# Kernel optimization log

Hardware: AMD Instinct MI355X
Metric: run time of the kernel (lower is better)

## Reference

```python
import jax, jax.numpy as jnp
import numpy as np

OBS = 256      # observation_space_size == state_vector_len
SV = 2047      # STATE_VECTORS = WMG_MAX_OBS
D = 256        # tfm_vec_size = 8 heads * 32 head_size
H = 8
HD = 32
L = 2          # TFM_NUM_LAYERS
FF = 1024      # TFM_HIDDEN_SIZE
ACH = 512      # AC_HIDDEN_LAYER_SIZE
A = 16         # action_space_size


def setup_inputs() -> dict:
    key = jax.random.key(0)
    ks = jax.random.split(key, 24)
    r = lambda k, s: (jax.random.normal(k, s, jnp.float32) * 0.02)
    inp = {
        "observation": jax.random.normal(ks[0], (OBS,), jnp.float32),
        "old_vectors": jax.random.normal(ks[1], (SV, OBS), jnp.float32),
        "W_core": r(ks[2], (OBS, D)), "b_core": jnp.zeros((D,), jnp.float32),
        # memo embedding takes cat(state_vec, age_onehot) of size OBS+SV
        "W_memo": r(ks[3], (OBS + SV, D)), "b_memo": jnp.zeros((D,), jnp.float32),
        "Wq": r(ks[4], (L, D, D)), "bq": jnp.zeros((L, D), jnp.float32),
        "Wk": r(ks[5], (L, D, D)), "bk": jnp.zeros((L, D), jnp.float32),
        "Wv": r(ks[6], (L, D, D)), "bv": jnp.zeros((L, D), jnp.float32),
        "Wo": r(ks[7], (L, D, D)), "bo": jnp.zeros((L, D), jnp.float32),
        "ln1_g": jnp.ones((L, D), jnp.float32), "ln1_b": jnp.zeros((L, D), jnp.float32),
        "ln2_g": jnp.ones((L, D), jnp.float32), "ln2_b": jnp.zeros((L, D), jnp.float32),
        "W_ff1": r(ks[8], (L, D, FF)), "b_ff1": jnp.zeros((L, FF), jnp.float32),
        "W_ff2": r(ks[9], (L, FF, D)), "b_ff2": jnp.zeros((L, D), jnp.float32),
        "aW1": r(ks[10], (D, ACH)), "ab1": jnp.zeros((ACH,), jnp.float32),
        "aW2": r(ks[11], (ACH, ACH)), "ab2": jnp.zeros((ACH,), jnp.float32),
        "aWo": r(ks[12], (ACH, A)), "abo": jnp.zeros((A,), jnp.float32),
        "cW1": r(ks[13], (D, ACH)), "cb1": jnp.zeros((ACH,), jnp.float32),
        "cW2": r(ks[14], (ACH, ACH)), "cb2": jnp.zeros((ACH,), jnp.float32),
        "cWo": r(ks[15], (ACH, 1)), "cbo": jnp.zeros((1,), jnp.float32),
    }
    return inp


def _ln(x, g, b, eps=1e-5):
    m = jnp.mean(x, axis=-1, keepdims=True)
    v = jnp.mean(jnp.square(x - m), axis=-1, keepdims=True)
    return (x - m) * jax.lax.rsqrt(v + eps) * g + b


def reference(observation, old_vectors, W_core, b_core, W_memo, b_memo,
              Wq, bq, Wk, bk, Wv, bv, Wo, bo,
              ln1_g, ln1_b, ln2_g, ln2_b, W_ff1, b_ff1, W_ff2, b_ff2,
              aW1, ab1, aW2, ab2, aWo, abo, cW1, cb1, cW2, cb2, cWo, cbo):
    # core embedding [D]
    emb0 = observation @ W_core + b_core
    # fused memo + age-onehot embedding: cat(vec_i, e_i) @ W_memo == vec_i @ W_memo[:OBS] + W_memo[OBS+i]
    memo_emb = old_vectors @ W_memo[:OBS] + W_memo[OBS:] + b_memo  # [SV, D]
    x = jnp.concatenate([emb0[None, :], memo_emb], axis=0)[None]   # [1, 1+SV, D]
    S = 1 + SV
    scale = 1.0 / np.sqrt(HD).astype(np.float32)
    for l in range(L):
        q = (x @ Wq[l] + bq[l]).reshape(1, S, H, HD)
        k = (x @ Wk[l] + bk[l]).reshape(1, S, H, HD)
        v = (x @ Wv[l] + bv[l]).reshape(1, S, H, HD)
        scores = jnp.einsum('bqhd,bkhd->bhqk', q, k) * scale       # [1,H,S,S]
        probs = jax.nn.softmax(scores, axis=-1)
        ctx = jnp.einsum('bhqk,bkhd->bqhd', probs, v).reshape(1, S, D)
        x = _ln(x + ctx @ Wo[l] + bo[l], ln1_g[l], ln1_b[l])
        h = jax.nn.gelu(x @ W_ff1[l] + b_ff1[l])
        x = _ln(x + h @ W_ff2[l] + b_ff2[l], ln2_g[l], ln2_b[l])
    t = x[:, 0, :]                                                 # [1, D]
    ha = jnp.tanh(jnp.tanh(t @ aW1 + ab1) @ aW2 + ab2)
    policy = ha @ aWo + abo                                        # [1, A] logits
    hc = jnp.tanh(jnp.tanh(t @ cW1 + cb1) @ cW2 + cb2)
    value_est = hc @ cWo + cbo                                     # [1, 1]
    # WMG_MAX_MEMOS == 0 path: new state vector is tanh(observation)
    new_vector = jnp.tanh(observation)                             # [OBS]
    return value_est, policy, new_vector
```

## Files before the change

kernel.cpp:

```cpp
#include <hip/hip_runtime.h>
#include <stdint.h>

typedef __attribute__((ext_vector_type(8))) short bf16x8;
typedef __attribute__((ext_vector_type(4))) float f32x4;

constexpr int kOBS = 256;
constexpr int kSEQ = 2048;
constexpr int kD   = 256;
constexpr int kHD  = 32;
constexpr int kFF  = 1024;
constexpr int kACH = 512;
constexpr int kA   = 16;

__device__ __forceinline__ unsigned short f2b(float f) {
  union { float f; unsigned int u; } v; v.f = f;
  unsigned int r = v.u + 0x7FFFu + ((v.u >> 16) & 1u);
  return (unsigned short)(r >> 16);
}

struct ConvTable {
  const float* src[14];
  int K[14];
  int N[14];
  int dst[14];
  int tstart[15];
};

__global__ __launch_bounds__(256) void k_convert(ConvTable tab,
                                                 unsigned short* __restrict__ wT) {
  __shared__ unsigned short lt[64][72];
  int b = blockIdx.x;
  int m = 0;
  while (b >= tab.tstart[m + 1]) m++;
  const int tloc = b - tab.tstart[m];
  const int N = tab.N[m], K = tab.K[m];
  const int ntile = N >> 6;
  const int k0 = (tloc / ntile) * 64, n0 = (tloc % ntile) * 64;
  const float* src = tab.src[m];
  const int tid = threadIdx.x;
  {
    const int r = tid >> 2, c16 = (tid & 3) * 16;
    const float* sp = src + (size_t)(k0 + r) * N + n0 + c16;
    #pragma unroll
    for (int j = 0; j < 16; j++) lt[r][c16 + j] = f2b(sp[j]);
  }
  __syncthreads();
  {
    const int n = tid >> 2, kc = (tid & 3) * 16;
    unsigned short* dp = wT + tab.dst[m] + (size_t)(n0 + n) * K + k0 + kc;
    unsigned short g[16];
    #pragma unroll
    for (int j = 0; j < 16; j++) g[j] = lt[kc + j][n];
    *(bf16x8*)dp = *(bf16x8*)&g[0];
    *(bf16x8*)(dp + 8) = *(bf16x8*)&g[8];
  }
}

__global__ __launch_bounds__(256) void k_row0(const float* __restrict__ obs,
                                              const float* __restrict__ Wc,
                                              const float* __restrict__ bc,
                                              float* __restrict__ xf,
                                              unsigned short* __restrict__ xb) {
  const int n = threadIdx.x;
  float a = bc[n];
  #pragma unroll 8
  for (int k = 0; k < kOBS; k++) a += obs[k] * Wc[k * kD + n];
  xf[n] = a;
  xb[n] = f2b(a);
}

template <int EPI, bool AF32>
__global__ __launch_bounds__(256) void k_gemmA(
    const void* __restrict__ Ap, int lda, int M, int K,
    const unsigned short* __restrict__ BT,
    const float* __restrict__ p0, const float* __restrict__ p1,
    const float* __restrict__ p2,
    void* __restrict__ o0, void* __restrict__ o1, void* __restrict__ o2) {
  __shared__ unsigned short Al[64][40];
  __shared__ unsigned short Bl[64][40];
  const int tid = threadIdx.x;
  const int w = tid >> 6, l = tid & 63, lg = l >> 4, lr = l & 15;
  const int m0 = blockIdx.x * 64, n0 = blockIdx.y * 64;
  const int sr = tid >> 2, sk = (tid & 3) * 8;
  f32x4 acc[4];
  #pragma unroll
  for (int c = 0; c < 4; c++)
    #pragma unroll
    for (int i = 0; i < 4; i++) acc[c][i] = 0.f;

  auto loadA = [&](int k0) -> bf16x8 {
    bf16x8 av;
    if (m0 + sr < M) {
      if constexpr (AF32) {
        const float* ap = (const float*)Ap + (size_t)(m0 + sr) * lda + k0 + sk;
        #pragma unroll
        for (int j = 0; j < 8; j++) av[j] = (short)f2b(ap[j]);
      } else {
        av = *(const bf16x8*)((const unsigned short*)Ap +
                              (size_t)(m0 + sr) * lda + k0 + sk);
      }
    } else {
      #pragma unroll
      for (int j = 0; j < 8; j++) av[j] = 0;
    }
    return av;
  };

  bf16x8 av = loadA(0);
  bf16x8 bv = *(const bf16x8*)(BT + (size_t)(n0 + sr) * K + sk);

  for (int k0 = 0; k0 < K; k0 += 32) {
    __syncthreads();
    *(bf16x8*)&Al[sr][sk] = av;
    *(bf16x8*)&Bl[sr][sk] = bv;
    __syncthreads();
    if (k0 + 32 < K) {
      av = loadA(k0 + 32);
      bv = *(const bf16x8*)(BT + (size_t)(n0 + sr) * K + k0 + 32 + sk);
    }
    bf16x8 af = *(bf16x8*)&Al[w * 16 + lr][8 * lg];
    #pragma unroll
    for (int c = 0; c < 4; c++) {
      bf16x8 bf = *(bf16x8*)&Bl[c * 16 + lr][8 * lg];
      acc[c] = __builtin_amdgcn_mfma_f32_16x16x32_bf16(af, bf, acc[c], 0, 0, 0);
    }
  }

  #pragma unroll
  for (int c = 0; c < 4; c++) {
    #pragma unroll
    for (int i = 0; i < 4; i++) {
      const int gr = m0 + w * 16 + 4 * lg + i;
      const int gc = n0 + c * 16 + lr;
      if (gr >= M) continue;
      float v = acc[c][i];
      if constexpr (EPI == 0) {
        v += p0[gc] + p1[(size_t)gr * kD + gc];
        ((float*)o0)[(size_t)(gr + 1) * kD + gc] = v;
        ((unsigned short*)o1)[(size_t)(gr + 1) * kD + gc] = f2b(v);
      } else if constexpr (EPI == 1) {
        const int t = gc >> 8, cc = gc & 255;
        const float* bp = (t == 0) ? p0 : (t == 1 ? p1 : p2);
        unsigned short* op = (t == 0) ? (unsigned short*)o0
                              : (t == 1 ? (unsigned short*)o1
                                        : (unsigned short*)o2);
        v += bp[cc];
        if (t == 0) v *= 0.17677669529663687f;
        op[(size_t)gr * kD + cc] = f2b(v);
      } else if constexpr (EPI == 2) {
        v += p0[gc];
        const float g =
            0.5f * v *
            (1.0f + tanhf(0.7978845608028654f * (v + 0.044715f * v * v * v)));
        ((unsigned short*)o0)[(size_t)gr * kFF + gc] = f2b(g);
      } else {
        v += p0[gc] + ((const float*)o1)[(size_t)gr * kD + gc];
        ((float*)o0)[(size_t)gr * kD + gc] = v;
      }
    }
  }
}

__global__ __launch_bounds__(256) void k_ln(const float* __restrict__ tin,
                                            const float* __restrict__ gam,
                                            const float* __restrict__ bet,
                                            float* __restrict__ xf,
                                            unsigned short* __restrict__ xb) {
  const int w = threadIdx.x >> 6, l = threadIdx.x & 63;
  const int row = blockIdx.x * 4 + w;
  f32x4 v = *(const f32x4*)(tin + (size_t)row * kD + l * 4);
  float s = v[0] + v[1] + v[2] + v[3];
  #pragma unroll
  for (int mm = 1; mm < 64; mm <<= 1) s += __shfl_xor(s, mm);
  const float mn = s * (1.0f / 256.0f);
  const float d0 = v[0] - mn, d1 = v[1] - mn, d2 = v[2] - mn, d3 = v[3] - mn;
  float s2 = d0 * d0 + d1 * d1 + d2 * d2 + d3 * d3;
  #pragma unroll
  for (int mm = 1; mm < 64; mm <<= 1) s2 += __shfl_xor(s2, mm);
  const float rstd = rsqrtf(s2 * (1.0f / 256.0f) + 1e-5f);
  f32x4 g4 = *(const f32x4*)(gam + l * 4);
  f32x4 b4 = *(const f32x4*)(bet + l * 4);
  f32x4 y;
  y[0] = d0 * rstd * g4[0] + b4[0];
  y[1] = d1 * rstd * g4[1] + b4[1];
  y[2] = d2 * rstd * g4[2] + b4[2];
  y[3] = d3 * rstd * g4[3] + b4[3];
  *(f32x4*)(xf + (size_t)row * kD + l * 4) = y;
  unsigned long long pk = (unsigned long long)f2b(y[0]) |
                          ((unsigned long long)f2b(y[1]) << 16) |
                          ((unsigned long long)f2b(y[2]) << 32) |
                          ((unsigned long long)f2b(y[3]) << 48);
  *(unsigned long long*)(xb + (size_t)row * kD + l * 4) = pk;
}

__global__ __launch_bounds__(256) void k_attn(const unsigned short* __restrict__ q,
                                              const unsigned short* __restrict__ k,
                                              const unsigned short* __restrict__ v,
                                              float* __restrict__ pacc,
                                              float* __restrict__ pml,
                                              int tpb) {
  __shared__ unsigned short Kl[64][40];
  __shared__ unsigned short Vt[32][72];
  __shared__ unsigned short Pl[4][16][72];
  const int tid = threadIdx.x;
  const int w = tid >> 6, l = tid & 63, lg = l >> 4, lr = l & 15;
  const int q0 = blockIdx.x * 64;
  const int hoff = blockIdx.y * kHD;
  const int sr = tid >> 2, sk = (tid & 3) * 8;
  const int t0 = blockIdx.z * tpb;

  const bf16x8 qf =
      *(const bf16x8*)(q + (size_t)(q0 + w * 16 + lr) * kD + hoff + 8 * lg);

  float m_[4], l_[4];
  f32x4 acc[2];
  #pragma unroll
  for (int i = 0; i < 4; i++) { m_[i] = -1e30f; l_[i] = 0.f; }
  #pragma unroll
  for (int dt = 0; dt < 2; dt++)
    #pragma unroll
    for (int i = 0; i < 4; i++) acc[dt][i] = 0.f;

  bf16x8 kreg = *(const bf16x8*)(k + (size_t)(t0 * 64 + sr) * kD + hoff + sk);
  bf16x8 vreg = *(const bf16x8*)(v + (size_t)(t0 * 64 + sr) * kD + hoff + sk);

  for (int t = 0; t < tpb; t++) {
    __syncthreads();
    *(bf16x8*)&Kl[sr][sk] = kreg;
    #pragma unroll
    for (int j = 0; j < 8; j++) Vt[sk + j][sr] = (unsigned short)vreg[j];
    __syncthreads();
    if (t + 1 < tpb) {
      const size_t nx = (size_t)((t0 + t + 1) * 64 + sr) * kD + hoff + sk;
      kreg = *(const bf16x8*)(k + nx);
      vreg = *(const bf16x8*)(v + nx);
    }
    f32x4 s[4];
    #pragma unroll
    for (int c = 0; c < 4; c++) {
      f32x4 z;
      #pragma unroll
      for (int i = 0; i < 4; i++) z[i] = 0.f;
      bf16x8 kf = *(bf16x8*)&Kl[c * 16 + lr][8 * lg];
      s[c] = __builtin_amdgcn_mfma_f32_16x16x32_bf16(qf, kf, z, 0, 0, 0);
    }
    float tm[4];
    #pragma unroll
    for (int i = 0; i < 4; i++)
      tm[i] = fmaxf(fmaxf(s[0][i], s[1][i]), fmaxf(s[2][i], s[3][i]));
    #pragma unroll
    for (int mm = 1; mm <= 8; mm <<= 1)
      #pragma unroll
      for (int i = 0; i < 4; i++) tm[i] = fmaxf(tm[i], __shfl_xor(tm[i], mm));
    float p[4][4], rs[4], corr[4];
    #pragma unroll
    for (int i = 0; i < 4; i++) {
      const float nm = fmaxf(m_[i], tm[i]);
      corr[i] = __expf(m_[i] - nm);
      m_[i] = nm;
      rs[i] = 0.f;
    }
    #pragma unroll
    for (int c = 0; c < 4; c++)
      #pragma unroll
      for (int i = 0; i < 4; i++) {
        p[c][i] = __expf(s[c][i] - m_[i]);
        rs[i] += p[c][i];
      }
    #pragma unroll
    for (int mm = 1; mm <= 8; mm <<= 1)
      #pragma unroll
      for (int i = 0; i < 4; i++) rs[i] += __shfl_xor(rs[i], mm);
    #pragma unroll
    for (int i = 0; i < 4; i++) {
      l_[i] = l_[i] * corr[i] + rs[i];
      acc[0][i] *= corr[i];
      acc[1][i] *= corr[i];
    }
    #pragma unroll
    for (int c = 0; c < 4; c++)
      #pragma unroll
      for (int i = 0; i < 4; i++)
        Pl[w][4 * lg + i][c * 16 + lr] = f2b(p[c][i]);
    __syncthreads();
    #pragma unroll
    for (int k2 = 0; k2 < 2; k2++) {
      bf16x8 pf = *(bf16x8*)&Pl[w][lr][k2 * 32 + 8 * lg];
      #pragma unroll
      for (int dt = 0; dt < 2; dt++) {
        bf16x8 vf = *(bf16x8*)&Vt[dt * 16 + lr][k2 * 32 + 8 * lg];
        acc[dt] = __builtin_amdgcn_mfma_f32_16x16x32_bf16(pf, vf, acc[dt], 0, 0, 0);
      }
    }
  }

  const int pb = blockIdx.z * 8 + blockIdx.y;
  float* pa = pacc + (size_t)pb * kSEQ * kHD;
  float* pm = pml + (size_t)pb * kSEQ * 2;
  #pragma unroll
  for (int dt = 0; dt < 2; dt++)
    #pragma unroll
    for (int i = 0; i < 4; i++) {
      const int gr = q0 + w * 16 + 4 * lg + i;
      pa[(size_t)gr * kHD + dt * 16 + lr] = acc[dt][i];
    }
  if (lr == 0) {
    #pragma unroll
    for (int i = 0; i < 4; i++) {
      const int gr = q0 + w * 16 + 4 * lg + i;
      float2 ml; ml.x = m_[i]; ml.y = l_[i];
      *(float2*)&pm[(size_t)gr * 2] = ml;
    }
  }
}

__global__ __launch_bounds__(256) void k_combine(const float* __restrict__ pacc,
                                                 const float* __restrict__ pml,
                                                 unsigned short* __restrict__ ctx,
                                                 int nsplit) {
  const int tid = threadIdx.x;
  const int d = tid & 31;
  const int g = blockIdx.x * 8 + (tid >> 5);
  const int h = g >> 11;
  const int row = g & 2047;
  float M = -1e30f;
  for (int s = 0; s < nsplit; s++)
    M = fmaxf(M, pml[((size_t)(s * 8 + h) * kSEQ + row) * 2]);
  float L = 0.f, o = 0.f;
  for (int s = 0; s < nsplit; s++) {
    const size_t pb = (size_t)(s * 8 + h) * kSEQ + row;
    const float2 ml = *(const float2*)&pml[pb * 2];
    const float e = __expf(ml.x - M);
    L += ml.y * e;
    o += pacc[pb * kHD + d] * e;
  }
  ctx[(size_t)row * kD + h * kHD + d] = f2b(o / L);
}

__global__ __launch_bounds__(256) void k_head1(const float* __restrict__ xf,
                                               const float* __restrict__ aW1,
                                               const float* __restrict__ ab1,
                                               const float* __restrict__ cW1,
                                               const float* __restrict__ cb1,
                                               float* __restrict__ h1) {
  __shared__ float tl[256];
  __shared__ float red[4][64];
  const int tid = threadIdx.x;
  tl[tid] = xf[tid];
  __syncthreads();
  const int jj = blockIdx.x * 64;
  const bool actor = jj < 512;
  const float* W = actor ? aW1 : cW1;
  const float* b = actor ? ab1 : cb1;
  const int j0 = actor ? jj : jj - 512;
  const int ks = tid >> 6, j = tid & 63;
  float s = 0.f;
  #pragma unroll 4
  for (int k2 = ks * 64; k2 < ks * 64 + 64; k2++)
    s += tl[k2] * W[(size_t)k2 * kACH + j0 + j];
  red[ks][j] = s;
  __syncthreads();
  if (tid < 64) {
    float t = red[0][tid] + red[1][tid] + red[2][tid] + red[3][tid] + b[j0 + tid];
    h1[jj + tid] = tanhf(t);
  }
}

__global__ __launch_bounds__(256) void k_head2(const float* __restrict__ h1,
                                               const float* __restrict__ aW2,
                                               const float* __restrict__ ab2,
                                               const float* __restrict__ cW2,
                                               const float* __restrict__ cb2,
                                               float* __restrict__ h2) {
  __shared__ float tl[512];
  __shared__ float red[4][64];
  const int tid = threadIdx.x;
  const int jj = blockIdx.x * 64;
  const bool actor = jj < 512;
  const float* hin = actor ? h1 : h1 + 512;
  tl[tid] = hin[tid];
  tl[tid + 256] = hin[tid + 256];
  __syncthreads();
  const float* W = actor ? aW2 : cW2;
  const float* b = actor ? ab2 : cb2;
  const int j0 = actor ? jj : jj - 512;
  const int ks = tid >> 6, j = tid & 63;
  float s = 0.f;
  #pragma unroll 4
  for (int k2 = ks * 128; k2 < ks * 128 + 128; k2++)
    s += tl[k2] * W[(size_t)k2 * kACH + j0 + j];
  red[ks][j] = s;
  __syncthreads();
  if (tid < 64) {
    float t = red[0][tid] + red[1][tid] + red[2][tid] + red[3][tid] + b[j0 + tid];
    h2[jj + tid] = tanhf(t);
  }
}

__global__ __launch_bounds__(256) void k_head3(const float* __restrict__ h2,
                                               const float* __restrict__ aWo,
                                               const float* __restrict__ abo,
                                               const float* __restrict__ cWo,
                                               const float* __restrict__ cbo,
                                               const float* __restrict__ obs,
                                               float* __restrict__ out) {
  __shared__ float ha[512], hc[512], vred[4];
  const int tid = threadIdx.x;
  ha[tid] = h2[tid];
  ha[tid + 256] = h2[tid + 256];
  hc[tid] = h2[512 + tid];
  hc[tid + 256] = h2[768 + tid];
  __syncthreads();
  const int g = tid >> 4, lane16 = tid & 15;
  float s = 0.f;
  for (int k2 = lane16 * 32; k2 < lane16 * 32 + 32; k2++)
    s += ha[k2] * aWo[(size_t)k2 * kA + g];
  #pragma unroll
  for (int mm = 1; mm <= 8; mm <<= 1) s += __shfl_xor(s, mm);
  if (lane16 == 0) out[1 + g] = s + abo[g];
  float vv = hc[tid] * cWo[tid] + hc[tid + 256] * cWo[tid + 256];
  #pragma unroll
  for (int mm = 1; mm <= 32; mm <<= 1) vv += __shfl_xor(vv, mm);
  if ((tid & 63) == 0) vred[tid >> 6] = vv;
  __syncthreads();
  if (tid == 0) out[0] = vred[0] + vred[1] + vred[2] + vred[3] + cbo[0];
  out[17 + tid] = tanhf(obs[tid]);
}

extern "C" void kernel_launch(void* const* d_in, const int* in_sizes, int n_in,
                              void* d_out, int out_size, void* d_ws, size_t ws_size,
                              hipStream_t stream) {
  const float* obs   = (const float*)d_in[0];
  const float* oldv  = (const float*)d_in[1];
  const float* Wcore = (const float*)d_in[2];
  const float* bcore = (const float*)d_in[3];
  const float* Wmemo = (const float*)d_in[4];
  const float* bmemo = (const float*)d_in[5];
  const float* Wq    = (const float*)d_in[6];
  const float* bq    = (const float*)d_in[7];
  const float* Wk    = (const float*)d_in[8];
  const float* bk    = (const float*)d_in[9];
  const float* Wv    = (const float*)d_in[10];
  const float* bv    = (const float*)d_in[11];
  const float* Wo    = (const float*)d_in[12];
  const float* bo    = (const float*)d_in[13];
  const float* ln1g  = (const float*)d_in[14];
  const float* ln1b  = (const float*)d_in[15];
  const float* ln2g  = (const float*)d_in[16];
  const float* ln2b  = (const float*)d_in[17];
  const float* Wff1  = (const float*)d_in[18];
  const float* bff1  = (const float*)d_in[19];
  const float* Wff2  = (const float*)d_in[20];
  const float* bff2  = (const float*)d_in[21];
  const float* aW1   = (const float*)d_in[22];
  const float* ab1   = (const float*)d_in[23];
  const float* aW2   = (const float*)d_in[24];
  const float* ab2   = (const float*)d_in[25];
  const float* aWo   = (const float*)d_in[26];
  const float* abo   = (const float*)d_in[27];
  const float* cW1   = (const float*)d_in[28];
  const float* cb1   = (const float*)d_in[29];
  const float* cW2   = (const float*)d_in[30];
  const float* cb2   = (const float*)d_in[31];
  const float* cWo   = (const float*)d_in[32];
  const float* cbo   = (const float*)d_in[33];

  char* ws = (char*)d_ws;
  float*          xf  = (float*)(ws + 0);
  unsigned short* xb  = (unsigned short*)(ws + (2u << 20));
  unsigned short* qb  = (unsigned short*)(ws + (3u << 20));
  unsigned short* kb  = (unsigned short*)(ws + (4u << 20));
  unsigned short* vb  = (unsigned short*)(ws + (5u << 20));
  unsigned short* ctb = (unsigned short*)(ws + (6u << 20));
  unsigned short* hb  = (unsigned short*)(ws + (7u << 20));
  float*          tmp = (float*)(ws + (11u << 20));
  float*          h1  = (float*)(ws + (13u << 20));
  float*          h2  = (float*)(ws + (13u << 20) + 4096);
  unsigned short* wT  = (unsigned short*)(ws + (13u << 20) + 16384);

  const size_t pacc_off = (size_t)17u << 20;
  int nsplit = 8;
  while (nsplit > 1 &&
         pacc_off + (size_t)nsplit * (8 * kSEQ * kHD * 4 + 8 * kSEQ * 2 * 4) >
             ws_size)
    nsplit >>= 1;
  float* pacc = (float*)(ws + pacc_off);
  float* pml  = (float*)(ws + pacc_off + (size_t)nsplit * 8 * kSEQ * kHD * 4);
  const int tpb = 32 / nsplit;

  const int oCore = 0, oMemo = 65536;
  int oQKV[2], oWoT[2], oFF1[2], oFF2[2];
  int cur = 131072;
  for (int l2 = 0; l2 < 2; l2++) {
    oQKV[l2] = cur; cur += 196608;
    oWoT[l2] = cur; cur += 65536;
    oFF1[l2] = cur; cur += 262144;
    oFF2[l2] = cur; cur += 262144;
  }

  ConvTable tab;
  int idx = 0, ts = 0;
  auto add = [&](const float* s, int K, int N, int dst) {
    tab.src[idx] = s; tab.K[idx] = K; tab.N[idx] = N; tab.dst[idx] = dst;
    tab.tstart[idx] = ts; ts += (K >> 6) * (N >> 6); idx++;
  };
  add(Wcore, 256, 256, oCore);
  add(Wmemo, 256, 256, oMemo);
  for (int l2 = 0; l2 < 2; l2++) {
    add(Wq + l2 * 65536, 256, 256, oQKV[l2]);
    add(Wk + l2 * 65536, 256, 256, oQKV[l2] + 65536);
    add(Wv + l2 * 65536, 256, 256, oQKV[l2] + 131072);
    add(Wo + l2 * 65536, 256, 256, oWoT[l2]);
    add(Wff1 + l2 * 262144, 256, 1024, oFF1[l2]);
    add(Wff2 + l2 * 262144, 1024, 256, oFF2[l2]);
  }
  tab.tstart[14] = ts;

  k_row0<<<1, 256, 0, stream>>>(obs, Wcore, bcore, xf, xb);
  k_convert<<<ts, 256, 0, stream>>>(tab, wT);
  k_gemmA<0, true><<<dim3(32, 4), 256, 0, stream>>>(
      oldv, 256, 2047, 256, wT + oMemo, bmemo, Wmemo + 65536, nullptr,
      xf, xb, nullptr);

  for (int l2 = 0; l2 < 2; l2++) {
    k_gemmA<1, false><<<dim3(32, 12), 256, 0, stream>>>(
        xb, 256, 2048, 256, wT + oQKV[l2],
        bq + l2 * 256, bk + l2 * 256, bv + l2 * 256, qb, kb, vb);
    k_attn<<<dim3(32, 8, nsplit), 256, 0, stream>>>(qb, kb, vb, pacc, pml, tpb);
    k_combine<<<2048, 256, 0, stream>>>(pacc, pml, ctb, nsplit);
    k_gemmA<3, false><<<dim3(32, 4), 256, 0, stream>>>(
        ctb, 256, 2048, 256, wT + oWoT[l2],
        bo + l2 * 256, nullptr, nullptr, tmp, xf, nullptr);
    k_ln<<<512, 256, 0, stream>>>(tmp, ln1g + l2 * 256, ln1b + l2 * 256, xf, xb);
    k_gemmA<2, false><<<dim3(32, 16), 256, 0, stream>>>(
        xb, 256, 2048, 256, wT + oFF1[l2],
        bff1 + l2 * 1024, nullptr, nullptr, hb, nullptr, nullptr);
    k_gemmA<3, false><<<dim3(32, 4), 256, 0, stream>>>(
        hb, 1024, 2048, 1024, wT + oFF2[l2],
        bff2 + l2 * 256, nullptr, nullptr, tmp, xf, nullptr);
    k_ln<<<512, 256, 0, stream>>>(tmp, ln2g + l2 * 256, ln2b + l2 * 256, xf, xb);
  }

  k_head1<<<16, 256, 0, stream>>>(xf, aW1, ab1, cW1, cb1, h1);
  k_head2<<<16, 256, 0, stream>>>(h1, aW2, ab2, cW2, cb2, h2);
  k_head3<<<1, 256, 0, stream>>>(h2, aWo, abo, cWo, cbo, obs, (float*)d_out);
}
```

Before: 227.4 us.

## Fuse the whole forward pass into one cooperative persistent megakernel

Replaces the chain of about 20 kernel launches with one cooperative persistent kernel whose phases are separated by grid syncs. It also folds the split-softmax combine into the Wo GEMM and merges each LayerNorm into the preceding GEMM epilogue, so the fp32 temporaries are never written out. The attention split factor drops from 8 to 4. This is meant to remove launch gaps and intermediate memory round-trips, at the cost of grid-wide barriers, a grid capped by occupancy, and a per-kernel fallback path if the cooperative launch fails.

```diff
diff --git a/kernel.cpp b/kernel.cpp
--- a/kernel.cpp
+++ b/kernel.cpp
@@ -1,10 +1,12 @@
 #include <hip/hip_runtime.h>
+#include <hip/hip_cooperative_groups.h>
 #include <stdint.h>
+
+namespace cg = cooperative_groups;
 
 typedef __attribute__((ext_vector_type(8))) short bf16x8;
 typedef __attribute__((ext_vector_type(4))) float f32x4;
 
-constexpr int kOBS = 256;
 constexpr int kSEQ = 2048;
 constexpr int kD   = 256;
 constexpr int kHD  = 32;
@@ -26,61 +28,74 @@
   int tstart[15];
 };
 
-__global__ __launch_bounds__(256) void k_convert(ConvTable tab,
-                                                 unsigned short* __restrict__ wT) {
-  __shared__ unsigned short lt[64][72];
-  int b = blockIdx.x;
-  int m = 0;
-  while (b >= tab.tstart[m + 1]) m++;
-  const int tloc = b - tab.tstart[m];
-  const int N = tab.N[m], K = tab.K[m];
-  const int ntile = N >> 6;
-  const int k0 = (tloc / ntile) * 64, n0 = (tloc % ntile) * 64;
-  const float* src = tab.src[m];
-  const int tid = threadIdx.x;
-  {
-    const int r = tid >> 2, c16 = (tid & 3) * 16;
-    const float* sp = src + (size_t)(k0 + r) * N + n0 + c16;
-    #pragma unroll
-    for (int j = 0; j < 16; j++) lt[r][c16 + j] = f2b(sp[j]);
-  }
-  __syncthreads();
-  {
-    const int n = tid >> 2, kc = (tid & 3) * 16;
-    unsigned short* dp = wT + tab.dst[m] + (size_t)(n0 + n) * K + k0 + kc;
-    unsigned short g[16];
-    #pragma unroll
-    for (int j = 0; j < 16; j++) g[j] = lt[kc + j][n];
-    *(bf16x8*)dp = *(bf16x8*)&g[0];
-    *(bf16x8*)(dp + 8) = *(bf16x8*)&g[8];
-  }
-}
-
-__global__ __launch_bounds__(256) void k_row0(const float* __restrict__ obs,
-                                              const float* __restrict__ Wc,
-                                              const float* __restrict__ bc,
-                                              float* __restrict__ xf,
-                                              unsigned short* __restrict__ xb) {
-  const int n = threadIdx.x;
-  float a = bc[n];
-  #pragma unroll 8
-  for (int k = 0; k < kOBS; k++) a += obs[k] * Wc[k * kD + n];
-  xf[n] = a;
-  xb[n] = f2b(a);
+union SharedU {
+  struct { unsigned short lt[64][72]; } cv;
+  struct { unsigned short Al[64][40]; unsigned short Bl[64][40]; } g64;
+  struct { unsigned short Kl[64][40]; unsigned short Vt[32][72];
+           unsigned short Pl[4][16][72]; } at;
+  struct { unsigned short As[16][264]; float2 red[4][16]; } lg;
+  struct { float tl[512]; float red[4][64]; } hd;
+  struct { float ha[512]; float hc[512]; float vred[4]; } h3;
+};
+
+struct MegaParams {
+  ConvTable tab;
+  const float *obs, *oldv, *Wcore, *bcore, *bmemo, *Wmemo2;
+  const float *bq, *bk, *bv, *bo, *ln1g, *ln1b, *ln2g, *ln2b, *bff1, *bff2;
+  const float *aW1, *ab1, *aW2, *ab2, *aWo, *abo;
+  const float *cW1, *cb1, *cW2, *cb2, *cWo, *cbo;
+  float* xf; unsigned short* xb;
+  unsigned short *qb, *kb, *vb, *hb, *wT;
+  float *pacc, *pml, *h1, *h2, *out;
+  int oMemo, oQKV[2], oWoT[2], oFF1[2], oFF2[2];
+  int convJobs, nsplit, tpb;
+};
+
+__device__ void ph_conv(const MegaParams& p, SharedU& sh) {
+  const int tid = threadIdx.x;
+  for (int job = blockIdx.x; job <= p.convJobs; job += gridDim.x) {
+    __syncthreads();
+    if (job == p.convJobs) {
+      float a = p.bcore[tid];
+      #pragma unroll 8
+      for (int k = 0; k < 256; k++) a += p.obs[k] * p.Wcore[k * kD + tid];
+      p.xf[tid] = a;
+      p.xb[tid] = f2b(a);
+      continue;
+    }
+    int m = 0;
+    while (job >= p.tab.tstart[m + 1]) m++;
+    const int tloc = job - p.tab.tstart[m];
+    const int N = p.tab.N[m], K = p.tab.K[m];
+    const int ntile = N >> 6;
+    const int k0 = (tloc / ntile) * 64, n0 = (tloc % ntile) * 64;
+    const float* src = p.tab.src[m];
+    {
+      const int r = tid >> 2, c16 = (tid & 3) * 16;
+      const float* sp = src + (size_t)(k0 + r) * N + n0 + c16;
+      #pragma unroll
+      for (int j = 0; j < 16; j++) sh.cv.lt[r][c16 + j] = f2b(sp[j]);
+    }
+    __syncthreads();
+    {
+      const int n = tid >> 2, kc = (tid & 3) * 16;
+      unsigned short* dp = p.wT + p.tab.dst[m] + (size_t)(n0 + n) * K + k0 + kc;
+      unsigned short g[16];
+      #pragma unroll
+      for (int j = 0; j < 16; j++) g[j] = sh.cv.lt[kc + j][n];
+      *(bf16x8*)dp = *(bf16x8*)&g[0];
+      *(bf16x8*)(dp + 8) = *(bf16x8*)&g[8];
+    }
+  }
 }
 
 template <int EPI, bool AF32>
-__global__ __launch_bounds__(256) void k_gemmA(
-    const void* __restrict__ Ap, int lda, int M, int K,
-    const unsigned short* __restrict__ BT,
-    const float* __restrict__ p0, const float* __restrict__ p1,
-    const float* __restrict__ p2,
-    void* __restrict__ o0, void* __restrict__ o1, void* __restrict__ o2) {
-  __shared__ unsigned short Al[64][40];
-  __shared__ unsigned short Bl[64][40];
+__device__ __forceinline__ void gemm64_job(
+    SharedU& sh, int m0, int n0, const void* Ap, int lda, int M, int K,
+    const unsigned short* BT, const float* p0, const float* p1,
+    const float* p2, void* o0, void* o1, void* o2) {
   const int tid = threadIdx.x;
   const int w = tid >> 6, l = tid & 63, lg = l >> 4, lr = l & 15;
-  const int m0 = blockIdx.x * 64, n0 = blockIdx.y * 64;
   const int sr = tid >> 2, sk = (tid & 3) * 8;
   f32x4 acc[4];
   #pragma unroll
@@ -111,17 +126,17 @@
 
   for (int k0 = 0; k0 < K; k0 += 32) {
     __syncthreads();
-    *(bf16x8*)&Al[sr][sk] = av;
-    *(bf16x8*)&Bl[sr][sk] = bv;
+    *(bf16x8*)&sh.g64.Al[sr][sk] = av;
+    *(bf16x8*)&sh.g64.Bl[sr][sk] = bv;
     __syncthreads();
     if (k0 + 32 < K) {
       av = loadA(k0 + 32);
       bv = *(const bf16x8*)(BT + (size_t)(n0 + sr) * K + k0 + 32 + sk);
     }
-    bf16x8 af = *(bf16x8*)&Al[w * 16 + lr][8 * lg];
+    bf16x8 af = *(bf16x8*)&sh.g64.Al[w * 16 + lr][8 * lg];
     #pragma unroll
     for (int c = 0; c < 4; c++) {
-      bf16x8 bf = *(bf16x8*)&Bl[c * 16 + lr][8 * lg];
+      bf16x8 bf = *(bf16x8*)&sh.g64.Bl[c * 16 + lr][8 * lg];
       acc[c] = __builtin_amdgcn_mfma_f32_16x16x32_bf16(af, bf, acc[c], 0, 0, 0);
     }
   }
@@ -147,67 +162,38 @@
         v += bp[cc];
         if (t == 0) v *= 0.17677669529663687f;
         op[(size_t)gr * kD + cc] = f2b(v);
-      } else if constexpr (EPI == 2) {
+      } else {
         v += p0[gc];
         const float g =
             0.5f * v *
             (1.0f + tanhf(0.7978845608028654f * (v + 0.044715f * v * v * v)));
         ((unsigned short*)o0)[(size_t)gr * kFF + gc] = f2b(g);
-      } else {
-        v += p0[gc] + ((const float*)o1)[(size_t)gr * kD + gc];
-        ((float*)o0)[(size_t)gr * kD + gc] = v;
-      }
-    }
-  }
-}
-
-__global__ __launch_bounds__(256) void k_ln(const float* __restrict__ tin,
-                                            const float* __restrict__ gam,
-                                            const float* __restrict__ bet,
-                                            float* __restrict__ xf,
-                                            unsigned short* __restrict__ xb) {
-  const int w = threadIdx.x >> 6, l = threadIdx.x & 63;
-  const int row = blockIdx.x * 4 + w;
-  f32x4 v = *(const f32x4*)(tin + (size_t)row * kD + l * 4);
-  float s = v[0] + v[1] + v[2] + v[3];
-  #pragma unroll
-  for (int mm = 1; mm < 64; mm <<= 1) s += __shfl_xor(s, mm);
-  const float mn = s * (1.0f / 256.0f);
-  const float d0 = v[0] - mn, d1 = v[1] - mn, d2 = v[2] - mn, d3 = v[3] - mn;
-  float s2 = d0 * d0 + d1 * d1 + d2 * d2 + d3 * d3;
-  #pragma unroll
-  for (int mm = 1; mm < 64; mm <<= 1) s2 += __shfl_xor(s2, mm);
-  const float rstd = rsqrtf(s2 * (1.0f / 256.0f) + 1e-5f);
-  f32x4 g4 = *(const f32x4*)(gam + l * 4);
-  f32x4 b4 = *(const f32x4*)(bet + l * 4);
-  f32x4 y;
-  y[0] = d0 * rstd * g4[0] + b4[0];
-  y[1] = d1 * rstd * g4[1] + b4[1];
-  y[2] = d2 * rstd * g4[2] + b4[2];
-  y[3] = d3 * rstd * g4[3] + b4[3];
-  *(f32x4*)(xf + (size_t)row * kD + l * 4) = y;
-  unsigned long long pk = (unsigned long long)f2b(y[0]) |
-                          ((unsigned long long)f2b(y[1]) << 16) |
-                          ((unsigned long long)f2b(y[2]) << 32) |
-                          ((unsigned long long)f2b(y[3]) << 48);
-  *(unsigned long long*)(xb + (size_t)row * kD + l * 4) = pk;
-}
-
-__global__ __launch_bounds__(256) void k_attn(const unsigned short* __restrict__ q,
-                                              const unsigned short* __restrict__ k,
-                                              const unsigned short* __restrict__ v,
-                                              float* __restrict__ pacc,
-                                              float* __restrict__ pml,
-                                              int tpb) {
-  __shared__ unsigned short Kl[64][40];
-  __shared__ unsigned short Vt[32][72];
-  __shared__ unsigned short Pl[4][16][72];
+      }
+    }
+  }
+}
+
+template <int EPI, bool AF32>
+__device__ void ph_gemm(SharedU& sh, const void* Ap, int lda, int M, int K,
+                        const unsigned short* BT, int Mtiles, int Ntiles,
+                        const float* p0, const float* p1, const float* p2,
+                        void* o0, void* o1, void* o2) {
+  const int njobs = Mtiles * Ntiles;
+  for (int job = blockIdx.x; job < njobs; job += gridDim.x) {
+    const int m0 = (job % Mtiles) * 64, n0 = (job / Mtiles) * 64;
+    gemm64_job<EPI, AF32>(sh, m0, n0, Ap, lda, M, K, BT, p0, p1, p2, o0, o1, o2);
+  }
+}
+
+__device__ void attn_job(SharedU& sh, int qb_, int h, int s, int tpb,
+                         const unsigned short* q, const unsigned short* k,
+                         const unsigned short* v, float* pacc, float* pml) {
   const int tid = threadIdx.x;
   const int w = tid >> 6, l = tid & 63, lg = l >> 4, lr = l & 15;
-  const int q0 = blockIdx.x * 64;
-  const int hoff = blockIdx.y * kHD;
+  const int q0 = qb_ * 64;
+  const int hoff = h * kHD;
   const int sr = tid >> 2, sk = (tid & 3) * 8;
-  const int t0 = blockIdx.z * tpb;
+  const int t0 = s * tpb;
 
   const bf16x8 qf =
       *(const bf16x8*)(q + (size_t)(q0 + w * 16 + lr) * kD + hoff + 8 * lg);
@@ -226,33 +212,33 @@
 
   for (int t = 0; t < tpb; t++) {
     __syncthreads();
-    *(bf16x8*)&Kl[sr][sk] = kreg;
-    #pragma unroll
-    for (int j = 0; j < 8; j++) Vt[sk + j][sr] = (unsigned short)vreg[j];
+    *(bf16x8*)&sh.at.Kl[sr][sk] = kreg;
+    #pragma unroll
+    for (int j = 0; j < 8; j++) sh.at.Vt[sk + j][sr] = (unsigned short)vreg[j];
     __syncthreads();
     if (t + 1 < tpb) {
       const size_t nx = (size_t)((t0 + t + 1) * 64 + sr) * kD + hoff + sk;
       kreg = *(const bf16x8*)(k + nx);
       vreg = *(const bf16x8*)(v + nx);
     }
-    f32x4 s[4];
+    f32x4 sc[4];
     #pragma unroll
     for (int c = 0; c < 4; c++) {
       f32x4 z;
       #pragma unroll
       for (int i = 0; i < 4; i++) z[i] = 0.f;
-      bf16x8 kf = *(bf16x8*)&Kl[c * 16 + lr][8 * lg];
-      s[c] = __builtin_amdgcn_mfma_f32_16x16x32_bf16(qf, kf, z, 0, 0, 0);
+      bf16x8 kf = *(bf16x8*)&sh.at.Kl[c * 16 + lr][8 * lg];
+      sc[c] = __builtin_amdgcn_mfma_f32_16x16x32_bf16(qf, kf, z, 0, 0, 0);
     }
     float tm[4];
     #pragma unroll
     for (int i = 0; i < 4; i++)
-      tm[i] = fmaxf(fmaxf(s[0][i], s[1][i]), fmaxf(s[2][i], s[3][i]));
+      tm[i] = fmaxf(fmaxf(sc[0][i], sc[1][i]), fmaxf(sc[2][i], sc[3][i]));
     #pragma unroll
     for (int mm = 1; mm <= 8; mm <<= 1)
       #pragma unroll
       for (int i = 0; i < 4; i++) tm[i] = fmaxf(tm[i], __shfl_xor(tm[i], mm));
-    float p[4][4], rs[4], corr[4];
+    float pv[4][4], rs[4], corr[4];
     #pragma unroll
     for (int i = 0; i < 4; i++) {
       const float nm = fmaxf(m_[i], tm[i]);
@@ -264,8 +250,8 @@
     for (int c = 0; c < 4; c++)
       #pragma unroll
       for (int i = 0; i < 4; i++) {
-        p[c][i] = __expf(s[c][i] - m_[i]);
-        rs[i] += p[c][i];
+        pv[c][i] = __expf(sc[c][i] - m_[i]);
+        rs[i] += pv[c][i];
       }
     #pragma unroll
     for (int mm = 1; mm <= 8; mm <<= 1)
@@ -281,20 +267,20 @@
     for (int c = 0; c < 4; c++)
       #pragma unroll
       for (int i = 0; i < 4; i++)
-        Pl[w][4 * lg + i][c * 16 + lr] = f2b(p[c][i]);
+        sh.at.Pl[w][4 * lg + i][c * 16 + lr] = f2b(pv[c][i]);
     __syncthreads();
     #pragma unroll
     for (int k2 = 0; k2 < 2; k2++) {
-      bf16x8 pf = *(bf16x8*)&Pl[w][lr][k2 * 32 + 8 * lg];
+      bf16x8 pf = *(bf16x8*)&sh.at.Pl[w][lr][k2 * 32 + 8 * lg];
       #pragma unroll
       for (int dt = 0; dt < 2; dt++) {
-        bf16x8 vf = *(bf16x8*)&Vt[dt * 16 + lr][k2 * 32 + 8 * lg];
+        bf16x8 vf = *(bf16x8*)&sh.at.Vt[dt * 16 + lr][k2 * 32 + 8 * lg];
         acc[dt] = __builtin_amdgcn_mfma_f32_16x16x32_bf16(pf, vf, acc[dt], 0, 0, 0);
       }
     }
   }
 
-  const int pb = blockIdx.z * 8 + blockIdx.y;
+  const int pb = s * 8 + h;
   float* pa = pacc + (size_t)pb * kSEQ * kHD;
   float* pm = pml + (size_t)pb * kSEQ * 2;
   #pragma unroll
@@ -314,118 +300,320 @@
   }
 }
 
-__global__ __launch_bounds__(256) void k_combine(const float* __restrict__ pacc,
-                                                 const float* __restrict__ pml,
-                                                 unsigned short* __restrict__ ctx,
-                                                 int nsplit) {
-  const int tid = threadIdx.x;
-  const int d = tid & 31;
-  const int g = blockIdx.x * 8 + (tid >> 5);
-  const int h = g >> 11;
-  const int row = g & 2047;
-  float M = -1e30f;
-  for (int s = 0; s < nsplit; s++)
-    M = fmaxf(M, pml[((size_t)(s * 8 + h) * kSEQ + row) * 2]);
-  float L = 0.f, o = 0.f;
-  for (int s = 0; s < nsplit; s++) {
-    const size_t pb = (size_t)(s * 8 + h) * kSEQ + row;
-    const float2 ml = *(const float2*)&pml[pb * 2];
-    const float e = __expf(ml.x - M);
-    L += ml.y * e;
-    o += pacc[pb * kHD + d] * e;
-  }
-  ctx[(size_t)row * kD + h * kHD + d] = f2b(o / L);
-}
-
-__global__ __launch_bounds__(256) void k_head1(const float* __restrict__ xf,
-                                               const float* __restrict__ aW1,
-                                               const float* __restrict__ ab1,
-                                               const float* __restrict__ cW1,
-                                               const float* __restrict__ cb1,
-                                               float* __restrict__ h1) {
-  __shared__ float tl[256];
-  __shared__ float red[4][64];
-  const int tid = threadIdx.x;
-  tl[tid] = xf[tid];
+__device__ void ph_attn(const MegaParams& p, SharedU& sh) {
+  const int njobs = 256 * p.nsplit;
+  for (int job = blockIdx.x; job < njobs; job += gridDim.x) {
+    const int qb_ = job & 31, h = (job >> 5) & 7, s = job >> 8;
+    attn_job(sh, qb_, h, s, p.tpb, p.qb, p.kb, p.vb, p.pacc, p.pml);
+  }
+}
+
+__device__ __forceinline__ void ln_write(SharedU& sh, float vloc[4][4], int r0,
+                                         const float* gam, const float* bet,
+                                         float* xf, unsigned short* xb) {
+  const int tid = threadIdx.x;
+  const int w = tid >> 6, l = tid & 63, lg = l >> 4, lr = l & 15;
+  float ps[4], ps2[4];
+  #pragma unroll
+  for (int i = 0; i < 4; i++) {
+    ps[i] = 0.f; ps2[i] = 0.f;
+    #pragma unroll
+    for (int c = 0; c < 4; c++) {
+      ps[i] += vloc[c][i];
+      ps2[i] += vloc[c][i] * vloc[c][i];
+    }
+  }
+  #pragma unroll
+  for (int mm = 1; mm <= 8; mm <<= 1)
+    #pragma unroll
+    for (int i = 0; i < 4; i++) {
+      ps[i] += __shfl_xor(ps[i], mm);
+      ps2[i] += __shfl_xor(ps2[i], mm);
+    }
+  if (lr == 0) {
+    #pragma unroll
+    for (int i = 0; i < 4; i++) {
+      float2 t; t.x = ps[i]; t.y = ps2[i];
+      sh.lg.red[w][4 * lg + i] = t;
+    }
+  }
   __syncthreads();
-  const int jj = blockIdx.x * 64;
-  const bool actor = jj < 512;
-  const float* W = actor ? aW1 : cW1;
-  const float* b = actor ? ab1 : cb1;
-  const int j0 = actor ? jj : jj - 512;
-  const int ks = tid >> 6, j = tid & 63;
-  float s = 0.f;
-  #pragma unroll 4
-  for (int k2 = ks * 64; k2 < ks * 64 + 64; k2++)
-    s += tl[k2] * W[(size_t)k2 * kACH + j0 + j];
-  red[ks][j] = s;
-  __syncthreads();
-  if (tid < 64) {
-    float t = red[0][tid] + red[1][tid] + red[2][tid] + red[3][tid] + b[j0 + tid];
-    h1[jj + tid] = tanhf(t);
-  }
-}
-
-__global__ __launch_bounds__(256) void k_head2(const float* __restrict__ h1,
-                                               const float* __restrict__ aW2,
-                                               const float* __restrict__ ab2,
-                                               const float* __restrict__ cW2,
-                                               const float* __restrict__ cb2,
-                                               float* __restrict__ h2) {
-  __shared__ float tl[512];
-  __shared__ float red[4][64];
-  const int tid = threadIdx.x;
-  const int jj = blockIdx.x * 64;
-  const bool actor = jj < 512;
-  const float* hin = actor ? h1 : h1 + 512;
-  tl[tid] = hin[tid];
-  tl[tid + 256] = hin[tid + 256];
-  __syncthreads();
-  const float* W = actor ? aW2 : cW2;
-  const float* b = actor ? ab2 : cb2;
-  const int j0 = actor ? jj : jj - 512;
-  const int ks = tid >> 6, j = tid & 63;
-  float s = 0.f;
-  #pragma unroll 4
-  for (int k2 = ks * 128; k2 < ks * 128 + 128; k2++)
-    s += tl[k2] * W[(size_t)k2 * kACH + j0 + j];
-  red[ks][j] = s;
-  __syncthreads();
-  if (tid < 64) {
-    float t = red[0][tid] + red[1][tid] + red[2][tid] + red[3][tid] + b[j0 + tid];
-    h2[jj + tid] = tanhf(t);
-  }
-}
-
-__global__ __launch_bounds__(256) void k_head3(const float* __restrict__ h2,
-                                               const float* __restrict__ aWo,
-                                               const float* __restrict__ abo,
-                                               const float* __restrict__ cWo,
-                                               const float* __restrict__ cbo,
-                                               const float* __restrict__ obs,
-                                               float* __restrict__ out) {
-  __shared__ float ha[512], hc[512], vred[4];
-  const int tid = threadIdx.x;
-  ha[tid] = h2[tid];
-  ha[tid + 256] = h2[tid + 256];
-  hc[tid] = h2[512 + tid];
-  hc[tid + 256] = h2[768 + tid];
-  __syncthreads();
-  const int g = tid >> 4, lane16 = tid & 15;
-  float s = 0.f;
-  for (int k2 = lane16 * 32; k2 < lane16 * 32 + 32; k2++)
-    s += ha[k2] * aWo[(size_t)k2 * kA + g];
   #pragma unroll
-  for (int mm = 1; mm <= 8; mm <<= 1) s += __shfl_xor(s, mm);
-  if (lane16 == 0) out[1 + g] = s + abo[g];
-  float vv = hc[tid] * cWo[tid] + hc[tid + 256] * cWo[tid + 256];
-  #pragma unroll
-  for (int mm = 1; mm <= 32; mm <<= 1) vv += __shfl_xor(vv, mm);
-  if ((tid & 63) == 0) vred[tid >> 6] = vv;
-  __syncthreads();
-  if (tid == 0) out[0] = vred[0] + vred[1] + vred[2] + vred[3] + cbo[0];
-  out[17 + tid] = tanhf(obs[tid]);
-}
+  for (int i = 0; i < 4; i++) {
+    const int ri = 4 * lg + i;
+    float sx = 0.f, sx2 = 0.f;
+    #pragma unroll
+    for (int ww = 0; ww < 4; ww++) {
+      float2 t = sh.lg.red[ww][ri];
+      sx += t.x; sx2 += t.y;
+    }
+    const float mean = sx * (1.0f / 256.0f);
+    const float var = sx2 * (1.0f / 256.0f) - mean * mean;
+    const float rstd = rsqrtf(var + 1e-5f);
+    const int gr = r0 + ri;
+    #pragma unroll
+    for (int c = 0; c < 4; c++) {
+      const int col = w * 64 + c * 16 + lr;
+      const float y = (vloc[c][i] - mean) * rstd * gam[col] + bet[col];
+      xf[(size_t)gr * kD + col] = y;
+      xb[(size_t)gr * kD + col] = f2b(y);
+    }
+  }
+}
+
+__device__ void ph_woln(const MegaParams& p, SharedU& sh, int lyr) {
+  const unsigned short* BT = p.wT + p.oWoT[lyr];
+  const float* bias = p.bo + lyr * kD;
+  const float* gam = p.ln1g + lyr * kD;
+  const float* bet = p.ln1b + lyr * kD;
+  const int tid = threadIdx.x;
+  const int w = tid >> 6, l = tid & 63, lg = l >> 4, lr = l & 15;
+  for (int job = blockIdx.x; job < 128; job += gridDim.x) {
+    const int r0 = job * 16;
+    __syncthreads();
+    {
+      const int row = r0 + (tid >> 4);
+      const int kc = (tid & 15) * 16;
+      const int h_ = kc >> 5;
+      float mx = -1e30f;
+      float mlm[4], mll[4];
+      for (int s2 = 0; s2 < p.nsplit; s2++) {
+        const float2 t =
+            *(const float2*)&p.pml[((size_t)(s2 * 8 + h_) * kSEQ + row) * 2];
+        mlm[s2] = t.x; mll[s2] = t.y;
+        mx = fmaxf(mx, t.x);
+      }
+      float L = 0.f, e[4];
+      for (int s2 = 0; s2 < p.nsplit; s2++) {
+        e[s2] = __expf(mlm[s2] - mx);
+        L += mll[s2] * e[s2];
+      }
+      const float inv = 1.0f / L;
+      const int d0 = kc & 31;
+      float o[16];
+      #pragma unroll
+      for (int j = 0; j < 16; j++) o[j] = 0.f;
+      for (int s2 = 0; s2 < p.nsplit; s2++) {
+        const float* pa =
+            p.pacc + ((size_t)(s2 * 8 + h_) * kSEQ + row) * kHD + d0;
+        const float es = e[s2];
+        #pragma unroll
+        for (int j = 0; j < 16; j++) o[j] += pa[j] * es;
+      }
+      unsigned short* dst = &sh.lg.As[tid >> 4][kc];
+      #pragma unroll
+      for (int j = 0; j < 16; j++) dst[j] = f2b(o[j] * inv);
+    }
+    __syncthreads();
+    f32x4 acc[4];
+    #pragma unroll
+    for (int c = 0; c < 4; c++)
+      #pragma unroll
+      for (int i = 0; i < 4; i++) acc[c][i] = 0.f;
+    #pragma unroll 2
+    for (int k0 = 0; k0 < 256; k0 += 32) {
+      bf16x8 af = *(bf16x8*)&sh.lg.As[lr][k0 + 8 * lg];
+      #pragma unroll
+      for (int c = 0; c < 4; c++) {
+        bf16x8 bf = *(const bf16x8*)(BT + (size_t)(w * 64 + c * 16 + lr) * 256 +
+                                     k0 + 8 * lg);
+        acc[c] = __builtin_amdgcn_mfma_f32_16x16x32_bf16(af, bf, acc[c], 0, 0, 0);
+      }
+    }
+    float vloc[4][4];
+    #pragma unroll
+    for (int c = 0; c < 4; c++)
+      #pragma unroll
+      for (int i = 0; i < 4; i++) {
+        const int col = w * 64 + c * 16 + lr;
+        const int gr = r0 + 4 * lg + i;
+        vloc[c][i] = acc[c][i] + bias[col] + p.xf[(size_t)gr * kD + col];
+      }
+    ln_write(sh, vloc, r0, gam, bet, p.xf, p.xb);
+  }
+}
+
+__device__ void ph_ff2ln(const MegaParams& p, SharedU& sh, int lyr) {
+  const unsigned short* BT = p.wT + p.oFF2[lyr];
+  const float* bias = p.bff2 + lyr * kD;
+  const float* gam = p.ln2g + lyr * kD;
+  const float* bet = p.ln2b + lyr * kD;
+  const int tid = threadIdx.x;
+  const int w = tid >> 6, l = tid & 63, lg = l >> 4, lr = l & 15;
+  for (int job = blockIdx.x; job < 128; job += gridDim.x) {
+    const int r0 = job * 16;
+    f32x4 acc[4];
+    #pragma unroll
+    for (int c = 0; c < 4; c++)
+      #pragma unroll
+      for (int i = 0; i < 4; i++) acc[c][i] = 0.f;
+    const int srow = tid >> 4, skc = (tid & 15) * 16;
+    for (int kc = 0; kc < 1024; kc += 256) {
+      __syncthreads();
+      const unsigned short* src = p.hb + (size_t)(r0 + srow) * kFF + kc + skc;
+      *(bf16x8*)&sh.lg.As[srow][skc] = *(const bf16x8*)src;
+      *(bf16x8*)&sh.lg.As[srow][skc + 8] = *(const bf16x8*)(src + 8);
+      __syncthreads();
+      #pragma unroll 2
+      for (int k0 = 0; k0 < 256; k0 += 32) {
+        bf16x8 af = *(bf16x8*)&sh.lg.As[lr][k0 + 8 * lg];
+        #pragma unroll
+        for (int c = 0; c < 4; c++) {
+          bf16x8 bf = *(const bf16x8*)(
+              BT + (size_t)(w * 64 + c * 16 + lr) * 1024 + kc + k0 + 8 * lg);
+          acc[c] = __builtin_amdgcn_mfma_f32_16x16x32_bf16(af, bf, acc[c], 0, 0, 0);
+        }
+      }
+    }
+    float vloc[4][4];
+    #pragma unroll
+    for (int c = 0; c < 4; c++)
+      #pragma unroll
+      for (int i = 0; i < 4; i++) {
+        const int col = w * 64 + c * 16 + lr;
+        const int gr = r0 + 4 * lg + i;
+        vloc[c][i] = acc[c][i] + bias[col] + p.xf[(size_t)gr * kD + col];
+      }
+    ln_write(sh, vloc, r0, gam, bet, p.xf, p.xb);
+  }
+}
+
+__device__ void ph_h1(const MegaParams& p, SharedU& sh) {
+  const int tid = threadIdx.x;
+  for (int job = blockIdx.x; job < 16; job += gridDim.x) {
+    __syncthreads();
+    sh.hd.tl[tid] = p.xf[tid];
+    __syncthreads();
+    const int jj = job * 64;
+    const bool actor = jj < 512;
+    const float* W = actor ? p.aW1 : p.cW1;
+    const float* b = actor ? p.ab1 : p.cb1;
+    const int j0 = actor ? jj : jj - 512;
+    const int ks = tid >> 6, j = tid & 63;
+    float s = 0.f;
+    #pragma unroll 4
+    for (int k2 = ks * 64; k2 < ks * 64 + 64; k2++)
+      s += sh.hd.tl[k2] * W[(size_t)k2 * kACH + j0 + j];
+    sh.hd.red[ks][j] = s;
+    __syncthreads();
+    if (tid < 64) {
+      float t = sh.hd.red[0][tid] + sh.hd.red[1][tid] + sh.hd.red[2][tid] +
+                sh.hd.red[3][tid] + b[j0 + tid];
+      p.h1[jj + tid] = tanhf(t);
+    }
+  }
+}
+
+__device__ void ph_h2(const MegaParams& p, SharedU& sh) {
+  const int tid = threadIdx.x;
+  for (int job = blockIdx.x; job < 16; job += gridDim.x) {
+    __syncthreads();
+    const int jj = job * 64;
+    const bool actor = jj < 512;
+    const float* hin = actor ? p.h1 : p.h1 + 512;
+    sh.hd.tl[tid] = hin[tid];
+    sh.hd.tl[tid + 256] = hin[tid + 256];
+    __syncthreads();
+    const float* W = actor ? p.aW2 : p.cW2;
+    const float* b = actor ? p.ab2 : p.cb2;
+    const int j0 = actor ? jj : jj - 512;
+    const int ks = tid >> 6, j = tid & 63;
+    float s = 0.f;
+    #pragma unroll 4
+    for (int k2 = ks * 128; k2 < ks * 128 + 128; k2++)
+      s += sh.hd.tl[k2] * W[(size_t)k2 * kACH + j0 + j];
+    sh.hd.red[ks][j] = s;
+    __syncthreads();
+    if (tid < 64) {
+      float t = sh.hd.red[0][tid] + sh.hd.red[1][tid] + sh.hd.red[2][tid] +
+                sh.hd.red[3][tid] + b[j0 + tid];
+      p.h2[jj + tid] = tanhf(t);
+    }
+  }
+}
+
+__device__ void ph_h3(const MegaParams& p, SharedU& sh) {
+  const int tid = threadIdx.x;
+  for (int job = blockIdx.x; job < 1; job += gridDim.x) {
+    __syncthreads();
+    sh.h3.ha[tid] = p.h2[tid];
+    sh.h3.ha[tid + 256] = p.h2[tid + 256];
+    sh.h3.hc[tid] = p.h2[512 + tid];
+    sh.h3.hc[tid + 256] = p.h2[768 + tid];
+    __syncthreads();
+    const int g = tid >> 4, lane16 = tid & 15;
+    float s = 0.f;
+    for (int k2 = lane16 * 32; k2 < lane16 * 32 + 32; k2++)
+      s += sh.h3.ha[k2] * p.aWo[(size_t)k2 * kA + g];
+    #pragma unroll
+    for (int mm = 1; mm <= 8; mm <<= 1) s += __shfl_xor(s, mm);
+    if (lane16 == 0) p.out[1 + g] = s + p.abo[g];
+    float vv = sh.h3.hc[tid] * p.cWo[tid] + sh.h3.hc[tid + 256] * p.cWo[tid + 256];
+    #pragma unroll
+    for (int mm = 1; mm <= 32; mm <<= 1) vv += __shfl_xor(vv, mm);
+    if ((tid & 63) == 0) sh.h3.vred[tid >> 6] = vv;
+    __syncthreads();
+    if (tid == 0)
+      p.out[0] = sh.h3.vred[0] + sh.h3.vred[1] + sh.h3.vred[2] + sh.h3.vred[3] +
+                 p.cbo[0];
+    p.out[17 + tid] = tanhf(p.obs[tid]);
+  }
+}
+
+__global__ __launch_bounds__(256, 4) void mega(MegaParams p) {
+  __shared__ SharedU sh;
+  cg::grid_group g = cg::this_grid();
+  ph_conv(p, sh);
+  g.sync();
+  ph_gemm<0, true>(sh, p.oldv, 256, 2047, 256, p.wT + p.oMemo, 32, 4,
+                   p.bmemo, p.Wmemo2, nullptr, p.xf, p.xb, nullptr);
+  g.sync();
+  for (int lyr = 0; lyr < 2; lyr++) {
+    ph_gemm<1, false>(sh, p.xb, 256, 2048, 256, p.wT + p.oQKV[lyr], 32, 12,
+                      p.bq + lyr * 256, p.bk + lyr * 256, p.bv + lyr * 256,
+                      p.qb, p.kb, p.vb);
+    g.sync();
+    ph_attn(p, sh);
+    g.sync();
+    ph_woln(p, sh, lyr);
+    g.sync();
+    ph_gemm<2, false>(sh, p.xb, 256, 2048, 256, p.wT + p.oFF1[lyr], 32, 16,
+                      p.bff1 + lyr * 1024, nullptr, nullptr, p.hb, nullptr,
+                      nullptr);
+    g.sync();
+    ph_ff2ln(p, sh, lyr);
+    g.sync();
+  }
+  ph_h1(p, sh);
+  g.sync();
+  ph_h2(p, sh);
+  g.sync();
+  ph_h3(p, sh);
+}
+
+__global__ __launch_bounds__(256) void gk_conv(MegaParams p) { __shared__ SharedU sh; ph_conv(p, sh); }
+__global__ __launch_bounds__(256) void gk_memo(MegaParams p) {
+  __shared__ SharedU sh;
+  ph_gemm<0, true>(sh, p.oldv, 256, 2047, 256, p.wT + p.oMemo, 32, 4,
+                   p.bmemo, p.Wmemo2, nullptr, p.xf, p.xb, nullptr);
+}
+__global__ __launch_bounds__(256) void gk_qkv(MegaParams p, int lyr) {
+  __shared__ SharedU sh;
+  ph_gemm<1, false>(sh, p.xb, 256, 2048, 256, p.wT + p.oQKV[lyr], 32, 12,
+                    p.bq + lyr * 256, p.bk + lyr * 256, p.bv + lyr * 256,
+                    p.qb, p.kb, p.vb);
+}
+__global__ __launch_bounds__(256) void gk_attn(MegaParams p) { __shared__ SharedU sh; ph_attn(p, sh); }
+__global__ __launch_bounds__(256) void gk_woln(MegaParams p, int lyr) { __shared__ SharedU sh; ph_woln(p, sh, lyr); }
+__global__ __launch_bounds__(256) void gk_ff1(MegaParams p, int lyr) {
+  __shared__ SharedU sh;
+  ph_gemm<2, false>(sh, p.xb, 256, 2048, 256, p.wT + p.oFF1[lyr], 32, 16,
+                    p.bff1 + lyr * 1024, nullptr, nullptr, p.hb, nullptr, nullptr);
+}
+__global__ __launch_bounds__(256) void gk_ff2ln(MegaParams p, int lyr) { __shared__ SharedU sh; ph_ff2ln(p, sh, lyr); }
+__global__ __launch_bounds__(256) void gk_h1(MegaParams p) { __shared__ SharedU sh; ph_h1(p, sh); }
+__global__ __launch_bounds__(256) void gk_h2(MegaParams p) { __shared__ SharedU sh; ph_h2(p, sh); }
+__global__ __launch_bounds__(256) void gk_h3(MegaParams p) { __shared__ SharedU sh; ph_h3(p, sh); }
 
 extern "C" void kernel_launch(void* const* d_in, const int* in_sizes, int n_in,
                               void* d_out, int out_size, void* d_ws, size_t ws_size,
@@ -452,96 +640,92 @@
   const float* bff1  = (const float*)d_in[19];
   const float* Wff2  = (const float*)d_in[20];
   const float* bff2  = (const float*)d_in[21];
-  const float* aW1   = (const float*)d_in[22];
-  const float* ab1   = (const float*)d_in[23];
-  const float* aW2   = (const float*)d_in[24];
-  const float* ab2   = (const float*)d_in[25];
-  const float* aWo   = (const float*)d_in[26];
-  const float* abo   = (const float*)d_in[27];
-  const float* cW1   = (const float*)d_in[28];
-  const float* cb1   = (const float*)d_in[29];
-  const float* cW2   = (const float*)d_in[30];
-  const float* cb2   = (const float*)d_in[31];
-  const float* cWo   = (const float*)d_in[32];
-  const float* cbo   = (const float*)d_in[33];
+
+  MegaParams P;
+  P.obs = obs; P.oldv = oldv; P.Wcore = Wcore; P.bcore = bcore;
+  P.bmemo = bmemo; P.Wmemo2 = Wmemo + 256 * 256;
+  P.bq = bq; P.bk = bk; P.bv = bv; P.bo = bo;
+  P.ln1g = ln1g; P.ln1b = ln1b; P.ln2g = ln2g; P.ln2b = ln2b;
+  P.bff1 = bff1; P.bff2 = bff2;
+  P.aW1 = (const float*)d_in[22]; P.ab1 = (const float*)d_in[23];
+  P.aW2 = (const float*)d_in[24]; P.ab2 = (const float*)d_in[25];
+  P.aWo = (const float*)d_in[26]; P.abo = (const float*)d_in[27];
+  P.cW1 = (const float*)d_in[28]; P.cb1 = (const float*)d_in[29];
+  P.cW2 = (const float*)d_in[30]; P.cb2 = (const float*)d_in[31];
+  P.cWo = (const float*)d_in[32]; P.cbo = (const float*)d_in[33];
 
   char* ws = (char*)d_ws;
-  float*          xf  = (float*)(ws + 0);
-  unsigned short* xb  = (unsigned short*)(ws + (2u << 20));
-  unsigned short* qb  = (unsigned short*)(ws + (3u << 20));
-  unsigned short* kb  = (unsigned short*)(ws + (4u << 20));
-  unsigned short* vb  = (unsigned short*)(ws + (5u << 20));
-  unsigned short* ctb = (unsigned short*)(ws + (6u << 20));
-  unsigned short* hb  = (unsigned short*)(ws + (7u << 20));
-  float*          tmp = (float*)(ws + (11u << 20));
-  float*          h1  = (float*)(ws + (13u << 20));
-  float*          h2  = (float*)(ws + (13u << 20) + 4096);
-  unsigned short* wT  = (unsigned short*)(ws + (13u << 20) + 16384);
-
-  const size_t pacc_off = (size_t)17u << 20;
-  int nsplit = 8;
+  P.xf = (float*)(ws + 0);
+  P.xb = (unsigned short*)(ws + (2u << 20));
+  P.qb = (unsigned short*)(ws + (3u << 20));
+  P.kb = (unsigned short*)(ws + (4u << 20));
+  P.vb = (unsigned short*)(ws + (5u << 20));
+  P.hb = (unsigned short*)(ws + (6u << 20));
+  P.h1 = (float*)(ws + (10u << 20));
+  P.h2 = (float*)(ws + (10u << 20) + 8192);
+  P.wT = (unsigned short*)(ws + (10u << 20) + 65536);
+  P.out = (float*)d_out;
+
+  int nsplit = 4;
+  const size_t paccOff = (size_t)14u << 20;
   while (nsplit > 1 &&
-         pacc_off + (size_t)nsplit * (8 * kSEQ * kHD * 4 + 8 * kSEQ * 2 * 4) >
-             ws_size)
+         paccOff + (size_t)nsplit * 8 * kSEQ * (kHD + 2) * 4 > ws_size)
     nsplit >>= 1;
-  float* pacc = (float*)(ws + pacc_off);
-  float* pml  = (float*)(ws + pacc_off + (size_t)nsplit * 8 * kSEQ * kHD * 4);
-  const int tpb = 32 / nsplit;
-
-  const int oCore = 0, oMemo = 65536;
-  int oQKV[2], oWoT[2], oFF1[2], oFF2[2];
-  int cur = 131072;
+  P.pacc = (float*)(ws + paccOff);
+  P.pml = (float*)(ws + paccOff + (size_t)nsplit * 8 * kSEQ * kHD * 4);
+  P.nsplit = nsplit;
+  P.tpb = 32 / nsplit;
+
+  P.oMemo = 0;
+  int cur = 65536;
   for (int l2 = 0; l2 < 2; l2++) {
-    oQKV[l2] = cur; cur += 196608;
-    oWoT[l2] = cur; cur += 65536;
-    oFF1[l2] = cur; cur += 262144;
-    oFF2[l2] = cur; cur += 262144;
-  }
-
-  ConvTable tab;
+    P.oQKV[l2] = cur; cur += 196608;
+    P.oWoT[l2] = cur; cur += 65536;
+    P.oFF1[l2] = cur; cur += 262144;
+    P.oFF2[l2] = cur; cur += 262144;
+  }
+
   int idx = 0, ts = 0;
   auto add = [&](const float* s, int K, int N, int dst) {
-    tab.src[idx] = s; tab.K[idx] = K; tab.N[idx] = N; tab.dst[idx] = dst;
-    tab.tstart[idx] = ts; ts += (K >> 6) * (N >> 6); idx++;
+    P.tab.src[idx] = s; P.tab.K[idx] = K; P.tab.N[idx] = N;
+    P.tab.dst[idx] = dst; P.tab.tstart[idx] = ts;
+    ts += (K >> 6) * (N >> 6); idx++;
   };
-  add(Wcore, 256, 256, oCore);
-  add(Wmemo, 256, 256, oMemo);
+  add(Wmemo, 256, 256, P.oMemo);
   for (int l2 = 0; l2 < 2; l2++) {
-    add(Wq + l2 * 65536, 256, 256, oQKV[l2]);
-    add(Wk + l2 * 65536, 256, 256, oQKV[l2] + 65536);
-    add(Wv + l2 * 65536, 256, 256, oQKV[l2] + 131072);
-    add(Wo + l2 * 65536, 256, 256, oWoT[l2]);
-    add(Wff1 + l2 * 262144, 256, 1024, oFF1[l2]);
-    add(Wff2 + l2 * 262144, 1024, 256, oFF2[l2]);
-  }
-  tab.tstart[14] = ts;
-
-  k_row0<<<1, 256, 0, stream>>>(obs, Wcore, bcore, xf, xb);
-  k_convert<<<ts, 256, 0, stream>>>(tab, wT);
-  k_gemmA<0, true><<<dim3(32, 4), 256, 0, stream>>>(
-      oldv, 256, 2047, 256, wT + oMemo, bmemo, Wmemo + 65536, nullptr,
-      xf, xb, nullptr);
-
-  for (int l2 = 0; l2 < 2; l2++) {
-    k_gemmA<1, false><<<dim3(32, 12), 256, 0, stream>>>(
-        xb, 256, 2048, 256, wT + oQKV[l2],
-        bq + l2 * 256, bk + l2 * 256, bv + l2 * 256, qb, kb, vb);
-    k_attn<<<dim3(32, 8, nsplit), 256, 0, stream>>>(qb, kb, vb, pacc, pml, tpb);
-    k_combine<<<2048, 256, 0, stream>>>(pacc, pml, ctb, nsplit);
-    k_gemmA<3, false><<<dim3(32, 4), 256, 0, stream>>>(
-        ctb, 256, 2048, 256, wT + oWoT[l2],
-        bo + l2 * 256, nullptr, nullptr, tmp, xf, nullptr);
-    k_ln<<<512, 256, 0, stream>>>(tmp, ln1g + l2 * 256, ln1b + l2 * 256, xf, xb);
-    k_gemmA<2, false><<<dim3(32, 16), 256, 0, stream>>>(
-        xb, 256, 2048, 256, wT + oFF1[l2],
-        bff1 + l2 * 1024, nullptr, nullptr, hb, nullptr, nullptr);
-    k_gemmA<3, false><<<dim3(32, 4), 256, 0, stream>>>(
-        hb, 1024, 2048, 1024, wT + oFF2[l2],
-        bff2 + l2 * 256, nullptr, nullptr, tmp, xf, nullptr);
-    k_ln<<<512, 256, 0, stream>>>(tmp, ln2g + l2 * 256, ln2b + l2 * 256, xf, xb);
-  }
-
-  k_head1<<<16, 256, 0, stream>>>(xf, aW1, ab1, cW1, cb1, h1);
-  k_head2<<<16, 256, 0, stream>>>(h1, aW2, ab2, cW2, cb2, h2);
-  k_head3<<<1, 256, 0, stream>>>(h2, aWo, abo, cWo, cbo, obs, (float*)d_out);
-}
+    add(Wq + l2 * 65536, 256, 256, P.oQKV[l2]);
+    add(Wk + l2 * 65536, 256, 256, P.oQKV[l2] + 65536);
+    add(Wv + l2 * 65536, 256, 256, P.oQKV[l2] + 131072);
+    add(Wo + l2 * 65536, 256, 256, P.oWoT[l2]);
+    add(Wff1 + l2 * 262144, 256, 1024, P.oFF1[l2]);
+    add(Wff2 + l2 * 262144, 1024, 256, P.oFF2[l2]);
+  }
+  P.tab.tstart[idx] = ts;
+  P.convJobs = ts;
+
+  int occ = 0;
+  hipOccupancyMaxActiveBlocksPerMultiprocessor(&occ, mega, 256, 0);
+  int G = occ * 256;
+  if (G > 1024) G = 1024;
+
+  bool coop = false;
+  if (G >= 64) {
+    void* kp[1] = {(void*)&P};
+    coop = hipLaunchCooperativeKernel((const void*)mega, dim3(G), dim3(256),
+                                      kp, 0, stream) == hipSuccess;
+  }
+  if (!coop) {
+    gk_conv<<<ts + 1, 256, 0, stream>>>(P);
+    gk_memo<<<128, 256, 0, stream>>>(P);
+    for (int lyr = 0; lyr < 2; lyr++) {
+      gk_qkv<<<384, 256, 0, stream>>>(P, lyr);
+      gk_attn<<<256 * nsplit, 256, 0, stream>>>(P);
+      gk_woln<<<128, 256, 0, stream>>>(P, lyr);
+      gk_ff1<<<512, 256, 0, stream>>>(P, lyr);
+      gk_ff2ln<<<128, 256, 0, stream>>>(P, lyr);
+    }
+    gk_h1<<<16, 256, 0, stream>>>(P);
+    gk_h2<<<16, 256, 0, stream>>>(P);
+    gk_h3<<<1, 256, 0, stream>>>(P);
+  }
+}
```

Result: slower. 719.4 us (+216.4%).
